# Optimization experiments

Measured on AMD Instinct MI355X. Metric: run time of the kernel, lower is better.

## Reference

```python
import jax, jax.numpy as jnp
import numpy as np

B, S, D, F = 4, 2048, 1024, 4096

def setup_inputs() -> dict:
    key = jax.random.key(0)
    ks = jax.random.split(key, 6)
    return {
        "x": jax.random.normal(ks[0], (B, S, D), jnp.float32),
        "Qw": jax.random.normal(ks[1], (D, D), jnp.float32) / 40,
        "Kw": jax.random.normal(ks[2], (D, D), jnp.float32) / 40,
        "Vw": jax.random.normal(ks[3], (D, D), jnp.float32) / 40,
        "w1": jax.random.normal(ks[4], (D, F), jnp.float32) / 40,
        "b1": jnp.zeros((F,), jnp.float32),
        "w2": jax.random.normal(ks[5], (F, D), jnp.float32) / 40,
        "b2": jnp.zeros((D,), jnp.float32),
        "gamma1": jnp.ones((D,), jnp.float32),
        "beta1": jnp.zeros((D,), jnp.float32),
        "gamma2": jnp.ones((D,), jnp.float32),
        "beta2": jnp.zeros((D,), jnp.float32),
    }

def _layernorm(x, gamma, beta):
    num = x - jnp.mean(x, axis=-1, keepdims=True)
    den = jnp.sqrt(jnp.var(x, axis=-1, keepdims=True) + 1e-05)
    return gamma * (num / den) + beta

def _attention(x, Qw, Kw, Vw):
    Q, K, V = x @ Qw, x @ Kw, x @ Vw
    d = x.shape[-1]
    s = x.shape[-2]
    mask = jnp.where(jnp.tril(jnp.ones((s, s))) == 0, -jnp.inf, 0.0)
    scores = Q @ jnp.swapaxes(K, -1, -2) / jnp.sqrt(d) + mask
    return jax.nn.softmax(scores, axis=-1) @ V

def reference(x, Qw, Kw, Vw, w1, b1, w2, b2, gamma1, beta1, gamma2, beta2):
    x = x + _attention(_layernorm(x, gamma1, beta1), Qw, Kw, Vw)
    h = _layernorm(x, gamma2, beta2)
    x = x + (jax.nn.relu(h @ w1 + b1) @ w2 + b2)
    return x
```

## Files before the change

kernel.cpp:

```cpp
#include <hip/hip_runtime.h>
#include <hip/hip_bf16.h>

#define B_ 4
#define S_ 2048
#define D_ 1024
#define F_ 4096

typedef short bf16x8 __attribute__((ext_vector_type(8)));
typedef float f32x4 __attribute__((ext_vector_type(4)));

static __device__ __forceinline__ unsigned short f2bf(float f) {
    union { float f; unsigned int u; } v; v.f = f;
    unsigned int u = v.u + 0x7FFF + ((v.u >> 16) & 1);
    return (unsigned short)(u >> 16);
}
static __device__ __forceinline__ float bf2f(unsigned short u) {
    union { unsigned int u; float f; } v; v.u = ((unsigned int)u) << 16;
    return v.f;
}

typedef const __attribute__((address_space(1))) unsigned int* gp_t;
typedef __attribute__((address_space(3))) unsigned int* lp_t;
static __device__ __forceinline__ void gld16(const unsigned short* g, unsigned short* l) {
    __builtin_amdgcn_global_load_lds((gp_t)g, (lp_t)l, 16, 0, 0);
}

#define WAIT_VM8() __builtin_amdgcn_s_waitcnt(0x0F78)
#define WAIT_VM0() __builtin_amdgcn_s_waitcnt(0x0F70)

__global__ __launch_bounds__(256) void k_transpose_f32_bf16(
    const float* __restrict__ in, unsigned short* __restrict__ out, int R, int C) {
    __shared__ float t[32][33];
    int c0 = blockIdx.x * 32, r0 = blockIdx.y * 32;
    int x = threadIdx.x, y = threadIdx.y;
#pragma unroll
    for (int i = 0; i < 4; i++)
        t[y + 8 * i][x] = in[(size_t)(r0 + y + 8 * i) * C + c0 + x];
    __syncthreads();
#pragma unroll
    for (int i = 0; i < 4; i++)
        out[(size_t)(c0 + y + 8 * i) * R + r0 + x] = f2bf(t[x][y + 8 * i]);
}

__global__ __launch_bounds__(256) void k_transpose_w3(
    const float* __restrict__ Qw, const float* __restrict__ Kw, const float* __restrict__ Vw,
    unsigned short* __restrict__ out) {
    __shared__ float t[32][33];
    int z = blockIdx.z;
    const float* in = (z == 0) ? Qw : (z == 1) ? Kw : Vw;
    out += (size_t)z * D_ * D_;
    int c0 = blockIdx.x * 32, r0 = blockIdx.y * 32;
    int x = threadIdx.x, y = threadIdx.y;
#pragma unroll
    for (int i = 0; i < 4; i++)
        t[y + 8 * i][x] = in[(size_t)(r0 + y + 8 * i) * D_ + c0 + x];
    __syncthreads();
#pragma unroll
    for (int i = 0; i < 4; i++)
        out[(size_t)(c0 + y + 8 * i) * D_ + r0 + x] = f2bf(t[x][y + 8 * i]);
}

__global__ __launch_bounds__(256) void k_transpose_bf16(
    const unsigned short* __restrict__ in, unsigned short* __restrict__ out,
    int ldin, int ldout, long long szin, long long szout) {
    __shared__ unsigned short t[32][33];
    in += (long long)blockIdx.z * szin;
    out += (long long)blockIdx.z * szout;
    int c0 = blockIdx.x * 32, r0 = blockIdx.y * 32;
    int x = threadIdx.x, y = threadIdx.y;
#pragma unroll
    for (int i = 0; i < 4; i++)
        t[y + 8 * i][x] = in[(size_t)(r0 + y + 8 * i) * ldin + c0 + x];
    __syncthreads();
#pragma unroll
    for (int i = 0; i < 4; i++)
        out[(size_t)(c0 + y + 8 * i) * ldout + r0 + x] = t[x][y + 8 * i];
}

__global__ __launch_bounds__(256) void k_layernorm(
    const float* __restrict__ x, const float* __restrict__ gamma,
    const float* __restrict__ beta, unsigned short* __restrict__ out) {
    int row = blockIdx.x;
    int t = threadIdx.x;
    const float* xr = x + (size_t)row * D_;
    float4 v = ((const float4*)xr)[t];
    float s = v.x + v.y + v.z + v.w;
    float q = v.x * v.x + v.y * v.y + v.z * v.z + v.w * v.w;
#pragma unroll
    for (int off = 32; off; off >>= 1) {
        s += __shfl_down(s, off);
        q += __shfl_down(q, off);
    }
    __shared__ float ls[4], lq[4];
    int wv = t >> 6;
    if ((t & 63) == 0) { ls[wv] = s; lq[wv] = q; }
    __syncthreads();
    if (t == 0) {
        float S = ls[0] + ls[1] + ls[2] + ls[3];
        float Q = lq[0] + lq[1] + lq[2] + lq[3];
        float mean = S * (1.0f / D_);
        float var = Q * (1.0f / D_) - mean * mean;
        ls[0] = mean; lq[0] = rsqrtf(var + 1e-5f);
    }
    __syncthreads();
    float mean = ls[0], rstd = lq[0];
    float4 g = ((const float4*)gamma)[t];
    float4 b = ((const float4*)beta)[t];
    ushort4 o;
    o.x = f2bf(g.x * (v.x - mean) * rstd + b.x);
    o.y = f2bf(g.y * (v.y - mean) * rstd + b.y);
    o.z = f2bf(g.z * (v.z - mean) * rstd + b.z);
    o.w = f2bf(g.w * (v.w - mean) * rstd + b.w);
    ((ushort4*)(out + (size_t)row * D_))[t] = o;
}

__global__ __launch_bounds__(256) void k_softmax(unsigned short* __restrict__ sp) {
    int r = blockIdx.x;
    int i = r & (S_ - 1);
    unsigned short* row = sp + (size_t)r * S_;
    int t = threadIdx.x;
    int valid = i + 1;
    float vals[8];
    float mx = -1e30f;
#pragma unroll
    for (int k = 0; k < 8; k++) {
        int j = t + k * 256;
        vals[k] = (j < valid) ? bf2f(row[j]) : -1e30f;
        mx = fmaxf(mx, vals[k]);
    }
#pragma unroll
    for (int off = 32; off; off >>= 1) mx = fmaxf(mx, __shfl_xor(mx, off));
    __shared__ float red[4];
    if ((t & 63) == 0) red[t >> 6] = mx;
    __syncthreads();
    mx = fmaxf(fmaxf(red[0], red[1]), fmaxf(red[2], red[3]));
    __syncthreads();
    float e[8];
    float sum = 0.f;
#pragma unroll
    for (int k = 0; k < 8; k++) {
        int j = t + k * 256;
        e[k] = (j < valid) ? __expf(vals[k] - mx) : 0.f;
        sum += e[k];
    }
#pragma unroll
    for (int off = 32; off; off >>= 1) sum += __shfl_xor(sum, off);
    if ((t & 63) == 0) red[t >> 6] = sum;
    __syncthreads();
    sum = red[0] + red[1] + red[2] + red[3];
    float inv = 1.0f / sum;
#pragma unroll
    for (int k = 0; k < 8; k++) {
        int j = t + k * 256;
        row[j] = f2bf(e[k] * inv);
    }
}

template <int EPI>
__global__ __launch_bounds__(256) void k_gemm_bt(
    const unsigned short* __restrict__ A, const unsigned short* __restrict__ Bt,
    void* __restrict__ Cv, const float* __restrict__ bias, const float* __restrict__ res,
    int K, int lda, int ldb, int ldc,
    long long sA, long long sB, long long sC, float scale, int klimit, int swz) {
    int bn, bm, z;
    if (swz > 0) {
        int GN = gridDim.x, GM = gridDim.y;
        int L = blockIdx.x + GN * (blockIdx.y + GM * blockIdx.z);
        int rows = gridDim.y * gridDim.z;
        int xcd = L & 7;
        int s = L >> 3;
        int bng = GN / swz;
        int rpg = rows * swz / 8;
        int xg = xcd % swz, yg = xcd / swz;
        int bnl = s % bng;
        int rl = s / bng;
        int row = yg * rpg + rl;
        bn = xg * bng + bnl;
        bm = row % GM;
        z = row / GM;
    } else {
        bn = blockIdx.x; bm = blockIdx.y; z = blockIdx.z;
    }
    if (EPI == 1 && bn > bm) return;
    A += (long long)z * sA;
    Bt += (long long)z * sB;
    long long coff = (long long)z * sC;
    float* Cf = (float*)Cv;
    unsigned short* Cb = (unsigned short*)Cv;

    __shared__ unsigned short As[2][2][128 * 32];
    __shared__ unsigned short Bs[2][2][128 * 32];

    int t = threadIdx.x;
    int l = t & 63, w = t >> 6;
    int wm = (w & 1) * 64, wn = (w >> 1) * 64;
    int lr = l & 15, lq = l >> 4;

    f32x4 acc[4][4];
#pragma unroll
    for (int i = 0; i < 4; i++)
#pragma unroll
        for (int j = 0; j < 4; j++) acc[i][j] = (f32x4){0.f, 0.f, 0.f, 0.f};

    int kend = K;
    if (klimit) { int ke = (bm + 1) * 128; kend = ke < K ? ke : K; }

    int sr = l >> 2;
    int sc = (l & 3) * 8;
    const unsigned short* gA0 = A + (size_t)(bm * 128 + w * 32 + sr) * lda + sc;
    const unsigned short* gA1 = gA0 + (size_t)16 * lda;
    const unsigned short* gB0 = Bt + (size_t)(bn * 128 + w * 32 + sr) * ldb + sc;
    const unsigned short* gB1 = gB0 + (size_t)16 * ldb;

    auto stage = [&](int buf, int k0) {
#pragma unroll
        for (int kc = 0; kc < 2; kc++) {
            int kk = k0 + kc * 32;
            gld16(gA0 + kk, &As[buf][kc][(w * 32) * 32]);
            gld16(gA1 + kk, &As[buf][kc][(w * 32 + 16) * 32]);
            gld16(gB0 + kk, &Bs[buf][kc][(w * 32) * 32]);
            gld16(gB1 + kk, &Bs[buf][kc][(w * 32 + 16) * 32]);
        }
    };

    int NB = kend >> 6;
    stage(0, 0);
    for (int it = 0; it < NB; it++) {
        int cur = it & 1;
        if (it + 1 < NB) {
            stage(1 - cur, (it + 1) * 64);
            WAIT_VM8();
        } else {
            WAIT_VM0();
        }
        __builtin_amdgcn_s_barrier();
#pragma unroll
        for (int kc = 0; kc < 2; kc++) {
            bf16x8 af[4], bf[4];
#pragma unroll
            for (int i = 0; i < 4; i++)
                af[i] = *(const bf16x8*)(&As[cur][kc][(wm + i * 16 + lr) * 32 + lq * 8]);
#pragma unroll
            for (int j = 0; j < 4; j++)
                bf[j] = *(const bf16x8*)(&Bs[cur][kc][(wn + j * 16 + lr) * 32 + lq * 8]);
#pragma unroll
            for (int i = 0; i < 4; i++)
#pragma unroll
                for (int j = 0; j < 4; j++)
                    acc[i][j] = __builtin_amdgcn_mfma_f32_16x16x32_bf16(af[i], bf[j], acc[i][j], 0, 0, 0);
        }
        __builtin_amdgcn_s_barrier();
    }

#pragma unroll
    for (int i = 0; i < 4; i++) {
        int mbase = bm * 128 + wm + i * 16 + lq * 4;
#pragma unroll
        for (int j = 0; j < 4; j++) {
            int n = bn * 128 + wn + j * 16 + lr;
#pragma unroll
            for (int r = 0; r < 4; r++) {
                int m = mbase + r;
                float v = acc[i][j][r];
                long long idx = coff + (long long)m * ldc + n;
                if (EPI == 0) {
                    Cb[idx] = f2bf(v);
                } else if (EPI == 1) {
                    Cb[idx] = f2bf(v * scale);
                } else if (EPI == 2) {
                    Cf[idx] = v + res[idx];
                } else if (EPI == 3) {
                    float u = v + bias[n];
                    Cb[idx] = f2bf(u > 0.f ? u : 0.f);
                } else {
                    Cf[idx] = v + bias[n] + res[idx];
                }
            }
        }
    }
}

extern "C" void kernel_launch(void* const* d_in, const int* in_sizes, int n_in,
                              void* d_out, int out_size, void* d_ws, size_t ws_size,
                              hipStream_t stream) {
    const float* x      = (const float*)d_in[0];
    const float* Qw     = (const float*)d_in[1];
    const float* Kw     = (const float*)d_in[2];
    const float* Vw     = (const float*)d_in[3];
    const float* w1     = (const float*)d_in[4];
    const float* b1     = (const float*)d_in[5];
    const float* w2     = (const float*)d_in[6];
    const float* b2     = (const float*)d_in[7];
    const float* gamma1 = (const float*)d_in[8];
    const float* beta1  = (const float*)d_in[9];
    const float* gamma2 = (const float*)d_in[10];
    const float* beta2  = (const float*)d_in[11];
    float* out = (float*)d_out;

    char* ws = (char*)d_ws;
    size_t off = 0;
    auto alloc = [&](size_t bytes) -> void* {
        void* p = ws + off;
        off += (bytes + 255) & ~(size_t)255;
        return p;
    };
    const size_t MN = (size_t)B_ * S_ * D_;
    unsigned short* xn     = (unsigned short*)alloc(MN * 2);
    unsigned short* scoreP = (unsigned short*)alloc((size_t)B_ * S_ * S_ * 2);
    unsigned short* qkv    = (unsigned short*)alloc((size_t)B_ * S_ * 3072 * 2);
    unsigned short* VT     = (unsigned short*)alloc(MN * 2);
    unsigned short* QKVwT  = (unsigned short*)alloc((size_t)3 * D_ * D_ * 2);
    unsigned short* w1T    = (unsigned short*)alloc((size_t)D_ * F_ * 2);
    unsigned short* w2T    = (unsigned short*)alloc((size_t)F_ * D_ * 2);
    unsigned short* mid = qkv;

    dim3 tb(32, 8);
    k_transpose_w3<<<dim3(D_ / 32, D_ / 32, 3), tb, 0, stream>>>(Qw, Kw, Vw, QKVwT);
    k_transpose_f32_bf16<<<dim3(F_ / 32, D_ / 32), tb, 0, stream>>>(w1, w1T, D_, F_);
    k_transpose_f32_bf16<<<dim3(D_ / 32, F_ / 32), tb, 0, stream>>>(w2, w2T, F_, D_);

    k_layernorm<<<B_ * S_, 256, 0, stream>>>(x, gamma1, beta1, xn);

    const int Mtok = B_ * S_;
    k_gemm_bt<0><<<dim3(3072 / 128, Mtok / 128), 256, 0, stream>>>(
        xn, QKVwT, qkv, nullptr, nullptr, D_, D_, D_, 3072, 0, 0, 0, 1.f, 0, 4);

    k_transpose_bf16<<<dim3(D_ / 32, S_ / 32, B_), tb, 0, stream>>>(
        qkv + 2048, VT, 3072, S_, (long long)S_ * 3072, (long long)D_ * S_);

    k_gemm_bt<1><<<dim3(S_ / 128, S_ / 128, B_), 256, 0, stream>>>(
        qkv, qkv + 1024, scoreP, nullptr, nullptr, D_, 3072, 3072, S_,
        (long long)S_ * 3072, (long long)S_ * 3072, (long long)S_ * S_, 0.03125f, 0, 4);

    k_softmax<<<B_ * S_, 256, 0, stream>>>(scoreP);

    k_gemm_bt<2><<<dim3(D_ / 128, S_ / 128, B_), 256, 0, stream>>>(
        scoreP, VT, out, nullptr, x, S_, S_, S_, D_,
        (long long)S_ * S_, (long long)D_ * S_, (long long)S_ * D_, 1.f, 1, 2);

    k_layernorm<<<B_ * S_, 256, 0, stream>>>(out, gamma2, beta2, xn);

    k_gemm_bt<3><<<dim3(F_ / 128, Mtok / 128), 256, 0, stream>>>(
        xn, w1T, mid, b1, nullptr, D_, D_, D_, F_, 0, 0, 0, 1.f, 0, 4);

    k_gemm_bt<4><<<dim3(D_ / 128, Mtok / 128), 256, 0, stream>>>(
        mid, w2T, out, b2, out, F_, F_, F_, D_, 0, 0, 0, 1.f, 0, 2);
}
```

Measured before the change: 492.6 us.

## Add 256x256-tile 8-wave GEMM with interleaved LDS staging for QKV, scores, FFN1

Adds a new GEMM kernel using 256x256 output tiles with 512 threads, double-buffered direct global-to-LDS loads split into half-tiles, and a four-phase schedule where each quarter of MFMAs overlaps with staging of the next k-block pieces, with setprio around compute. It replaces the 128x128 kernel for the QKV projection, the causal score GEMM (skipping upper-triangle tiles), and the first FFN GEMM. Larger tiles raise arithmetic intensity and cut global traffic, at the cost of fewer blocks, much larger LDS (128KB) and register use, and coarser causal-skip granularity.

```diff
diff --git a/kernel.cpp b/kernel.cpp
--- a/kernel.cpp
+++ b/kernel.cpp
@@ -26,6 +26,7 @@
 }
 
 #define WAIT_VM8() __builtin_amdgcn_s_waitcnt(0x0F78)
+#define WAIT_VM6() __builtin_amdgcn_s_waitcnt(0x0F76)
 #define WAIT_VM0() __builtin_amdgcn_s_waitcnt(0x0F70)
 
 __global__ __launch_bounds__(256) void k_transpose_f32_bf16(
@@ -280,6 +281,177 @@
     }
 }
 
+template <int EPI>
+__global__ __launch_bounds__(512, 2) void k_gemm256(
+    const unsigned short* __restrict__ A, const unsigned short* __restrict__ Bt,
+    void* __restrict__ Cv, const float* __restrict__ bias, const float* __restrict__ res,
+    int K, int lda, int ldb, int ldc,
+    long long sA, long long sB, long long sC, float scale, int klimit) {
+    int bn = blockIdx.x, bm = blockIdx.y, z = blockIdx.z;
+    if (EPI == 1 && bn > bm) return;
+    A += (long long)z * sA;
+    Bt += (long long)z * sB;
+    long long coff = (long long)z * sC;
+    float* Cf = (float*)Cv;
+    unsigned short* Cb = (unsigned short*)Cv;
+
+    __shared__ unsigned short As[2][2][128 * 64];
+    __shared__ unsigned short Bs[2][2][128 * 64];
+
+    int t = threadIdx.x;
+    int l = t & 63, w = t >> 6;
+    int wmh = w >> 2;
+    int wnh = (w >> 1) & 1;
+    int bnl = (w & 1) * 64;
+    int lr = l & 15, lq = l >> 4;
+    int sx = ((lr >> 2) & 1) << 4;
+    int foff = lr * 64 + ((lq * 8) ^ sx);
+
+    f32x4 acc[8][4];
+#pragma unroll
+    for (int i = 0; i < 8; i++)
+#pragma unroll
+        for (int j = 0; j < 4; j++) acc[i][j] = (f32x4){0.f, 0.f, 0.f, 0.f};
+
+    int kend = K;
+    if (klimit) { int ke = (bm + 1) * 256; kend = ke < K ? ke : K; }
+    int NB = kend >> 6;
+
+    int grow = l >> 3;
+    int gcol = ((l & 7) * 8) ^ (((l >> 5) & 1) << 4);
+    const unsigned short* gA = A + (size_t)(bm * 256 + w * 16 + grow) * lda + gcol;
+    const unsigned short* gB = Bt + (size_t)(bn * 256 + w * 16 + grow) * ldb + gcol;
+
+    auto stageA = [&](int buf, int half, int k0) {
+        const unsigned short* g = gA + (size_t)(half * 128) * lda + k0;
+        unsigned short* s = &As[buf][half][(w * 16) * 64];
+        gld16(g, s);
+        gld16(g + (size_t)8 * lda, s + 8 * 64);
+    };
+    auto stageB = [&](int buf, int half, int k0) {
+        const unsigned short* g = gB + (size_t)(half * 128) * ldb + k0;
+        unsigned short* s = &Bs[buf][half][(w * 16) * 64];
+        gld16(g, s);
+        gld16(g + (size_t)8 * ldb, s + 8 * 64);
+    };
+
+    stageA(0, 0, 0); stageA(0, 1, 0);
+    stageB(0, 0, 0); stageB(0, 1, 0);
+    int kp = (NB > 1) ? 64 : 0;
+    stageB(1, 0, kp); stageB(1, 1, kp); stageA(1, 0, kp);
+    WAIT_VM6();
+    __builtin_amdgcn_s_barrier();
+
+    bf16x8 aF0[2][4], aF1[2][4], bF[2][4];
+
+    for (int j = 0; j < NB; j++) {
+        int b = j & 1;
+        int k1 = ((j + 1 < NB) ? (j + 1) : (NB - 1)) << 6;
+        int k2 = ((j + 2 < NB) ? (j + 2) : (NB - 1)) << 6;
+        const unsigned short* Ah = &As[b][wmh][0];
+        const unsigned short* Bh = &Bs[b][wnh][0];
+
+#pragma unroll
+        for (int kc = 0; kc < 2; kc++) {
+#pragma unroll
+            for (int f = 0; f < 4; f++)
+                bF[kc][f] = *(const bf16x8*)(Bh + (bnl + f * 16) * 64 + kc * 32 + foff);
+#pragma unroll
+            for (int f = 0; f < 4; f++)
+                aF0[kc][f] = *(const bf16x8*)(Ah + (f * 16) * 64 + kc * 32 + foff);
+        }
+        stageA(b ^ 1, 1, k1);
+        __builtin_amdgcn_s_barrier();
+        __builtin_amdgcn_s_setprio(1);
+#pragma unroll
+        for (int kc = 0; kc < 2; kc++)
+#pragma unroll
+            for (int i = 0; i < 4; i++)
+#pragma unroll
+                for (int jn = 0; jn < 2; jn++)
+                    acc[i][jn] = __builtin_amdgcn_mfma_f32_16x16x32_bf16(
+                        aF0[kc][i], bF[kc][jn], acc[i][jn], 0, 0, 0);
+        __builtin_amdgcn_s_setprio(0);
+        __builtin_amdgcn_s_barrier();
+
+#pragma unroll
+        for (int kc = 0; kc < 2; kc++)
+#pragma unroll
+            for (int f = 0; f < 4; f++)
+                aF1[kc][f] = *(const bf16x8*)(Ah + (64 + f * 16) * 64 + kc * 32 + foff);
+        stageB(b, 0, k2);
+        __builtin_amdgcn_s_barrier();
+        __builtin_amdgcn_s_setprio(1);
+#pragma unroll
+        for (int kc = 0; kc < 2; kc++)
+#pragma unroll
+            for (int i = 0; i < 4; i++)
+#pragma unroll
+                for (int jn = 0; jn < 2; jn++)
+                    acc[4 + i][jn] = __builtin_amdgcn_mfma_f32_16x16x32_bf16(
+                        aF1[kc][i], bF[kc][jn], acc[4 + i][jn], 0, 0, 0);
+        __builtin_amdgcn_s_setprio(0);
+        __builtin_amdgcn_s_barrier();
+
+        stageB(b, 1, k2);
+        __builtin_amdgcn_s_barrier();
+        __builtin_amdgcn_s_setprio(1);
+#pragma unroll
+        for (int kc = 0; kc < 2; kc++)
+#pragma unroll
+            for (int i = 0; i < 4; i++)
+#pragma unroll
+                for (int jn = 0; jn < 2; jn++)
+                    acc[4 + i][2 + jn] = __builtin_amdgcn_mfma_f32_16x16x32_bf16(
+                        aF1[kc][i], bF[kc][2 + jn], acc[4 + i][2 + jn], 0, 0, 0);
+        __builtin_amdgcn_s_setprio(0);
+        __builtin_amdgcn_s_barrier();
+
+        stageA(b, 0, k2);
+        WAIT_VM6();
+        __builtin_amdgcn_s_barrier();
+        __builtin_amdgcn_s_setprio(1);
+#pragma unroll
+        for (int kc = 0; kc < 2; kc++)
+#pragma unroll
+            for (int i = 0; i < 4; i++)
+#pragma unroll
+                for (int jn = 0; jn < 2; jn++)
+                    acc[i][2 + jn] = __builtin_amdgcn_mfma_f32_16x16x32_bf16(
+                        aF0[kc][i], bF[kc][2 + jn], acc[i][2 + jn], 0, 0, 0);
+        __builtin_amdgcn_s_setprio(0);
+        __builtin_amdgcn_s_barrier();
+    }
+    WAIT_VM0();
+
+#pragma unroll
+    for (int i = 0; i < 8; i++) {
+        int mbase = bm * 256 + wmh * 128 + i * 16 + lq * 4;
+#pragma unroll
+        for (int jn = 0; jn < 4; jn++) {
+            int n = bn * 256 + (w & 3) * 64 + jn * 16 + lr;
+#pragma unroll
+            for (int r = 0; r < 4; r++) {
+                int m = mbase + r;
+                float v = acc[i][jn][r];
+                long long idx = coff + (long long)m * ldc + n;
+                if (EPI == 0) {
+                    Cb[idx] = f2bf(v);
+                } else if (EPI == 1) {
+                    Cb[idx] = f2bf(v * scale);
+                } else if (EPI == 2) {
+                    Cf[idx] = v + res[idx];
+                } else if (EPI == 3) {
+                    float u = v + bias[n];
+                    Cb[idx] = f2bf(u > 0.f ? u : 0.f);
+                } else {
+                    Cf[idx] = v + bias[n] + res[idx];
+                }
+            }
+        }
+    }
+}
+
 extern "C" void kernel_launch(void* const* d_in, const int* in_sizes, int n_in,
                               void* d_out, int out_size, void* d_ws, size_t ws_size,
                               hipStream_t stream) {
@@ -322,15 +494,15 @@
     k_layernorm<<<B_ * S_, 256, 0, stream>>>(x, gamma1, beta1, xn);
 
     const int Mtok = B_ * S_;
-    k_gemm_bt<0><<<dim3(3072 / 128, Mtok / 128), 256, 0, stream>>>(
-        xn, QKVwT, qkv, nullptr, nullptr, D_, D_, D_, 3072, 0, 0, 0, 1.f, 0, 4);
+    k_gemm256<0><<<dim3(3072 / 256, Mtok / 256), 512, 0, stream>>>(
+        xn, QKVwT, qkv, nullptr, nullptr, D_, D_, D_, 3072, 0, 0, 0, 1.f, 0);
 
     k_transpose_bf16<<<dim3(D_ / 32, S_ / 32, B_), tb, 0, stream>>>(
         qkv + 2048, VT, 3072, S_, (long long)S_ * 3072, (long long)D_ * S_);
 
-    k_gemm_bt<1><<<dim3(S_ / 128, S_ / 128, B_), 256, 0, stream>>>(
+    k_gemm256<1><<<dim3(S_ / 256, S_ / 256, B_), 512, 0, stream>>>(
         qkv, qkv + 1024, scoreP, nullptr, nullptr, D_, 3072, 3072, S_,
-        (long long)S_ * 3072, (long long)S_ * 3072, (long long)S_ * S_, 0.03125f, 0, 4);
+        (long long)S_ * 3072, (long long)S_ * 3072, (long long)S_ * S_, 0.03125f, 0);
 
     k_softmax<<<B_ * S_, 256, 0, stream>>>(scoreP);
 
@@ -340,8 +512,8 @@
 
     k_layernorm<<<B_ * S_, 256, 0, stream>>>(out, gamma2, beta2, xn);
 
-    k_gemm_bt<3><<<dim3(F_ / 128, Mtok / 128), 256, 0, stream>>>(
-        xn, w1T, mid, b1, nullptr, D_, D_, D_, F_, 0, 0, 0, 1.f, 0, 4);
+    k_gemm256<3><<<dim3(F_ / 256, Mtok / 256), 512, 0, stream>>>(
+        xn, w1T, mid, b1, nullptr, D_, D_, D_, F_, 0, 0, 0, 1.f, 0);
 
     k_gemm_bt<4><<<dim3(D_ / 128, Mtok / 128), 256, 0, stream>>>(
         mid, w2T, out, b2, out, F_, F_, F_, D_, 0, 0, 0, 1.f, 0, 2);
```

Measured after the change: 494.3 us. About the same (+0.3%).
